# Performance work log

Hardware: AMD Instinct MI355X
Metric: run time of the kernel (lower is better)

## Reference

```python
import jax, jax.numpy as jnp
import numpy as np

B, T, I, H = 512, 512, 8, 256


def setup_inputs() -> dict:
    key = jax.random.key(0)
    ks = jax.random.split(key, 4)
    x = jax.random.normal(ks[0], (B, T, I), dtype=jnp.float32)
    W_ih = jax.random.normal(ks[1], (3 * H, I), dtype=jnp.float32) * 0.1
    W_hh = jax.random.normal(ks[2], (3 * H, H), dtype=jnp.float32) * 0.05
    b_ih = jnp.zeros((3 * H,), dtype=jnp.float32)
    b_hh = jnp.zeros((3 * H,), dtype=jnp.float32)
    W_lin = jax.random.normal(ks[3], (1, H), dtype=jnp.float32) * 0.05
    b_lin = jnp.zeros((1,), dtype=jnp.float32)
    return {"x": x, "W_ih": W_ih, "W_hh": W_hh, "b_ih": b_ih,
            "b_hh": b_hh, "W_lin": W_lin, "b_lin": b_lin,
            "pred_length": T}


def reference(x, W_ih, W_hh, b_ih, b_hh, W_lin, b_lin, pred_length):
    # GRU (pred_type='full'): emit lin_usage(h_t) at every timestep.
    Hd = W_hh.shape[1]

    def step(h, x_t):
        gi = x_t @ W_ih.T + b_ih          # [B, 3H]
        gh = h @ W_hh.T + b_hh            # [B, 3H]
        i_r, i_z, i_n = jnp.split(gi, 3, axis=-1)
        h_r, h_z, h_n = jnp.split(gh, 3, axis=-1)
        r = jax.nn.sigmoid(i_r + h_r)
        z = jax.nn.sigmoid(i_z + h_z)
        n = jnp.tanh(i_n + r * h_n)
        h_new = (1.0 - z) * n + z * h
        pred = h_new @ W_lin.T + b_lin    # [B, 1]
        return h_new, pred

    h0 = jnp.zeros((x.shape[0], Hd), dtype=x.dtype)
    _, preds = jax.lax.scan(step, h0, jnp.swapaxes(x, 0, 1))  # preds: [T, B, 1]
    return jnp.swapaxes(preds, 0, 1)                          # [B, T, 1]
```

## Files before the change

### kernel.cpp

```cpp
#include <hip/hip_runtime.h>

#define TT 512
#define II 8
#define HH 256
#define ST 296
#define RR 8
#define NB 64
#define XSR 136

typedef _Float16 h4_t  __attribute__((ext_vector_type(4)));
typedef _Float16 h8_t  __attribute__((ext_vector_type(8)));
typedef float    f32x2 __attribute__((ext_vector_type(2)));
typedef float    f32x4 __attribute__((ext_vector_type(4)));

__device__ inline h8_t cvt8(const float* __restrict__ p, float s) {
    h8_t r;
#pragma unroll
    for (int i = 0; i < 8; ++i) r[i] = (_Float16)(p[i] * s);
    return r;
}

__global__ void __launch_bounds__(512, 2) gru_kernel(
    const float* __restrict__ x,    const float* __restrict__ W_ih,
    const float* __restrict__ W_hh, const float* __restrict__ b_ih,
    const float* __restrict__ b_hh, const float* __restrict__ W_lin,
    const float* __restrict__ b_lin, float* __restrict__ out)
{
    __shared__ _Float16 hbuf[2][16][ST];
    __shared__ h8_t wz1buf[8 * 8 * 64];
    __shared__ h8_t wn1buf[8 * 8 * 64];
    __shared__ _Float16 xstage[2][RR][XSR];
    __shared__ float predbuf[2][RR][64];

    const int tid  = threadIdx.x;
    const int w    = tid >> 6;
    const int lane = tid & 63;
    const int q    = lane >> 4;
    const int r15  = lane & 15;
    const int row0 = blockIdx.x * RR;

    const float sRZ = -1.44269504088896340736f;
    const float sN  =  2.88539008177792681472f;

    const int c0 = w * 32 + r15;
    const int c1 = c0 + 16;

    h8_t wfR0[8], wfZ0[8], wfN0[8], wfR1[8];
#pragma unroll
    for (int s = 0; s < 8; ++s) {
        const int k0 = s * 32 + q * 8;
        wfR0[s] = cvt8(W_hh + (size_t)(c0)       * HH + k0, sRZ);
        wfZ0[s] = cvt8(W_hh + (size_t)(256 + c0) * HH + k0, sRZ);
        wfN0[s] = cvt8(W_hh + (size_t)(512 + c0) * HH + k0, sN);
        wfR1[s] = cvt8(W_hh + (size_t)(c1)       * HH + k0, sRZ);
        wz1buf[(w * 8 + s) * 64 + lane] = cvt8(W_hh + (size_t)(256 + c1) * HH + k0, sRZ);
        wn1buf[(w * 8 + s) * 64 + lane] = cvt8(W_hh + (size_t)(512 + c1) * HH + k0, sN);
    }
    h4_t xfR[2], xfZ[2], xfN[2];
#pragma unroll
    for (int g = 0; g < 2; ++g) {
        const int cR = g ? c1 : c0;
#pragma unroll
        for (int j = 0; j < 4; ++j) {
            const int kp = q * 4 + j;
            float vR = 0.f, vZ = 0.f, vN = 0.f;
            if (kp < 8) {
                vR = W_ih[(cR)       * II + kp] * sRZ;
                vZ = W_ih[(256 + cR) * II + kp] * sRZ;
                vN = W_ih[(512 + cR) * II + kp] * sN;
            } else if (kp == 8) {
                vR = (b_ih[cR]       + b_hh[cR])       * sRZ;
                vZ = (b_ih[256 + cR] + b_hh[256 + cR]) * sRZ;
                vN = b_ih[512 + cR] * sN;
            }
            xfR[g][j] = (_Float16)vR; xfZ[g][j] = (_Float16)vZ; xfN[g][j] = (_Float16)vN;
        }
    }
    const bool hi = (lane >= 32);
    const float bhnp = (hi ? b_hh[512 + c1] : b_hh[512 + c0]) * sN;
    const float blin = b_lin[0];
    const float wl0 = W_lin[lane * 4 + 0], wl1 = W_lin[lane * 4 + 1];
    const float wl2 = W_lin[lane * 4 + 2], wl3 = W_lin[lane * 4 + 3];

    const h4_t bias4 = {(_Float16)1.f, (_Float16)0.f, (_Float16)0.f, (_Float16)0.f};
    const h4_t zero4 = {(_Float16)0.f, (_Float16)0.f, (_Float16)0.f, (_Float16)0.f};

    for (int i = tid; i < 2 * 16 * ST; i += 512) (&hbuf[0][0][0])[i] = (_Float16)0.f;
    {
        const int rr_ = tid >> 6, f2 = (tid & 63) * 2;
        const f32x2 v = *(const f32x2*)(x + (size_t)(row0 + rr_) * TT * II + f2);
        xstage[0][rr_][f2]     = (_Float16)v[0];
        xstage[0][rr_][f2 + 1] = (_Float16)v[1];
    }
    __syncthreads();

    const h8_t* __restrict__ wz_lane = &wz1buf[w * 8 * 64 + lane];
    const h8_t* __restrict__ wn_lane = &wn1buf[w * 8 * 64 + lane];

    f32x4 hreg = {0.f, 0.f, 0.f, 0.f};
    const f32x4 z4 = {0.f, 0.f, 0.f, 0.f};

    const int rb   = (q & 1) * 4;
    const int colp = hi ? c1 : c0;

    f32x2 xpre = {0.f, 0.f};
    const int xrow = tid >> 6, xf2 = (tid & 63) * 2;

    for (int t = 0; t < TT; ++t) {
        const int cur = t & 1, nxt = cur ^ 1;
        const int win = (t >> 4) & 1;

        if ((t & 15) == 0 && t + 16 < TT) {
            xpre = *(const f32x2*)(x + ((size_t)(row0 + xrow) * TT + (t + 16)) * II + xf2);
        }

        const _Float16* hb = &hbuf[cur][r15][0];
        const h4_t xa = *(const h4_t*)&xstage[win][r15 & 7][(t & 15) * 8 + (q & 1) * 4];
        const h4_t a2 = (q < 2) ? xa : ((q == 2) ? bias4 : zero4);
        f32x4 accR0 = __builtin_amdgcn_mfma_f32_16x16x16f16(a2, xfR[0], z4, 0, 0, 0);
        f32x4 accZ0 = __builtin_amdgcn_mfma_f32_16x16x16f16(a2, xfZ[0], z4, 0, 0, 0);
        f32x4 gin0  = __builtin_amdgcn_mfma_f32_16x16x16f16(a2, xfN[0], z4, 0, 0, 0);
        f32x4 accR1 = __builtin_amdgcn_mfma_f32_16x16x16f16(a2, xfR[1], z4, 0, 0, 0);
        f32x4 accZ1 = __builtin_amdgcn_mfma_f32_16x16x16f16(a2, xfZ[1], z4, 0, 0, 0);
        f32x4 gin1  = __builtin_amdgcn_mfma_f32_16x16x16f16(a2, xfN[1], z4, 0, 0, 0);
        f32x4 accN0 = z4, accN1 = z4;
#pragma unroll
        for (int s = 0; s < 8; ++s) {
            const h8_t a  = *(const h8_t*)(hb + s * 32 + q * 8);
            const h8_t wz = wz_lane[s * 64];
            const h8_t wn = wn_lane[s * 64];
            accR0 = __builtin_amdgcn_mfma_f32_16x16x32_f16(a, wfR0[s], accR0, 0, 0, 0);
            accZ0 = __builtin_amdgcn_mfma_f32_16x16x32_f16(a, wfZ0[s], accZ0, 0, 0, 0);
            accN0 = __builtin_amdgcn_mfma_f32_16x16x32_f16(a, wfN0[s], accN0, 0, 0, 0);
            accR1 = __builtin_amdgcn_mfma_f32_16x16x32_f16(a, wfR1[s], accR1, 0, 0, 0);
            accZ1 = __builtin_amdgcn_mfma_f32_16x16x32_f16(a, wz,     accZ1, 0, 0, 0);
            accN1 = __builtin_amdgcn_mfma_f32_16x16x32_f16(a, wn,     accN1, 0, 0, 0);
        }

        if (t > 0) {
            const h4_t hv4 = *(const h4_t*)&hbuf[cur][w][lane * 4];
            float s0 = (float)hv4[0] * wl0 + (float)hv4[1] * wl1
                     + (float)hv4[2] * wl2 + (float)hv4[3] * wl3;
#pragma unroll
            for (int m = 32; m >= 1; m >>= 1) s0 += __shfl_xor(s0, m, 64);
            if (lane == 0) predbuf[((t - 1) >> 6) & 1][w][(t - 1) & 63] = s0 + blin;
        }

        _Float16* hw = &hbuf[nxt][rb][colp];
#pragma unroll
        for (int j = 0; j < 4; ++j) {
            const float vR = hi ? accR1[j] : accR0[j];
            const float vZ = hi ? accZ1[j] : accZ0[j];
            const float vN = hi ? accN1[j] : accN0[j];
            const float vG = hi ? gin1[j]  : gin0[j];
            const float rr = __builtin_amdgcn_rcpf(1.f + __builtin_amdgcn_exp2f(vR));
            const float zz = __builtin_amdgcn_rcpf(1.f + __builtin_amdgcn_exp2f(vZ));
            const float u  = vG + rr * (vN + bhnp);
            const float nn = 1.f - 2.f * __builtin_amdgcn_rcpf(1.f + __builtin_amdgcn_exp2f(u));
            const float hv = nn + zz * (hreg[j] - nn);
            hreg[j] = hv;
            const _Float16 hh = (_Float16)hv;
            hw[j * ST]          = hh;
            hw[j * ST + 8 * ST] = hh;
        }

        if ((t & 15) == 15 && t + 1 < TT) {
            _Float16* xd = &xstage[win ^ 1][xrow][xf2];
            xd[0] = (_Float16)xpre[0];
            xd[1] = (_Float16)xpre[1];
        }

        __syncthreads();

        if ((t & 63) == 0 && t > 0) {
            const int pb = ((t >> 6) & 1) ^ 1;
            out[(size_t)(row0 + (tid >> 6)) * TT + (t - 64) + (tid & 63)] =
                predbuf[pb][tid >> 6][tid & 63];
        }
    }

    {
        const h4_t hv4 = *(const h4_t*)&hbuf[TT & 1][w][lane * 4];
        float s0 = (float)hv4[0] * wl0 + (float)hv4[1] * wl1
                 + (float)hv4[2] * wl2 + (float)hv4[3] * wl3;
#pragma unroll
        for (int m = 32; m >= 1; m >>= 1) s0 += __shfl_xor(s0, m, 64);
        if (lane == 0) predbuf[1][w][63] = s0 + blin;
    }
    __syncthreads();
    out[(size_t)(row0 + (tid >> 6)) * TT + 448 + (tid & 63)] =
        predbuf[1][tid >> 6][tid & 63];
}

extern "C" void kernel_launch(void* const* d_in, const int* in_sizes, int n_in,
                              void* d_out, int out_size, void* d_ws, size_t ws_size,
                              hipStream_t stream) {
    const float* x     = (const float*)d_in[0];
    const float* W_ih  = (const float*)d_in[1];
    const float* W_hh  = (const float*)d_in[2];
    const float* b_ih  = (const float*)d_in[3];
    const float* b_hh  = (const float*)d_in[4];
    const float* W_lin = (const float*)d_in[5];
    const float* b_lin = (const float*)d_in[6];
    float* out = (float*)d_out;
    gru_kernel<<<NB, 512, 0, stream>>>(x, W_ih, W_hh, b_ih, b_hh, W_lin, b_lin, out);
}
```

Measured before the change: 886.5 us.

## Halve block to 256 threads with each wave computing 64 hidden columns

Workgroups shrink from 8 waves to 4, and each wave now processes two 32-column groups in sequence, doubling its MFMA work per step. More recurrent weights stay in registers (10 of 12 fragment sets), so fewer weights are fetched from LDS each step. The intent is to make the per-step __syncthreads cheaper with fewer waves and to cut LDS weight traffic. The cost is much higher register pressure and a longer serial MFMA chain per wave. With one block per CU and only 64 blocks, each CU holds just 4 waves, which leaves little latency hiding.

```diff
diff --git a/kernel.cpp b/kernel.cpp
--- a/kernel.cpp
+++ b/kernel.cpp
@@ -20,15 +20,15 @@
     return r;
 }
 
-__global__ void __launch_bounds__(512, 2) gru_kernel(
+__global__ void __launch_bounds__(256, 1) gru_kernel(
     const float* __restrict__ x,    const float* __restrict__ W_ih,
     const float* __restrict__ W_hh, const float* __restrict__ b_ih,
     const float* __restrict__ b_hh, const float* __restrict__ W_lin,
     const float* __restrict__ b_lin, float* __restrict__ out)
 {
     __shared__ _Float16 hbuf[2][16][ST];
-    __shared__ h8_t wz1buf[8 * 8 * 64];
-    __shared__ h8_t wn1buf[8 * 8 * 64];
+    __shared__ h8_t wn1buf[4 * 8 * 64];
+    __shared__ h8_t wn3buf[4 * 8 * 64];
     __shared__ _Float16 xstage[2][RR][XSR];
     __shared__ float predbuf[2][RR][64];
 
@@ -42,10 +42,13 @@
     const float sRZ = -1.44269504088896340736f;
     const float sN  =  2.88539008177792681472f;
 
-    const int c0 = w * 32 + r15;
+    const int c0 = w * 64 + r15;
     const int c1 = c0 + 16;
-
-    h8_t wfR0[8], wfZ0[8], wfN0[8], wfR1[8];
+    const int c2 = c0 + 32;
+    const int c3 = c0 + 48;
+
+    h8_t wfR0[8], wfZ0[8], wfN0[8], wfR1[8], wfZ1[8];
+    h8_t wfR2[8], wfZ2[8], wfN2[8], wfR3[8], wfZ3[8];
 #pragma unroll
     for (int s = 0; s < 8; ++s) {
         const int k0 = s * 32 + q * 8;
@@ -53,13 +56,20 @@
         wfZ0[s] = cvt8(W_hh + (size_t)(256 + c0) * HH + k0, sRZ);
         wfN0[s] = cvt8(W_hh + (size_t)(512 + c0) * HH + k0, sN);
         wfR1[s] = cvt8(W_hh + (size_t)(c1)       * HH + k0, sRZ);
-        wz1buf[(w * 8 + s) * 64 + lane] = cvt8(W_hh + (size_t)(256 + c1) * HH + k0, sRZ);
+        wfZ1[s] = cvt8(W_hh + (size_t)(256 + c1) * HH + k0, sRZ);
+        wfR2[s] = cvt8(W_hh + (size_t)(c2)       * HH + k0, sRZ);
+        wfZ2[s] = cvt8(W_hh + (size_t)(256 + c2) * HH + k0, sRZ);
+        wfN2[s] = cvt8(W_hh + (size_t)(512 + c2) * HH + k0, sN);
+        wfR3[s] = cvt8(W_hh + (size_t)(c3)       * HH + k0, sRZ);
+        wfZ3[s] = cvt8(W_hh + (size_t)(256 + c3) * HH + k0, sRZ);
         wn1buf[(w * 8 + s) * 64 + lane] = cvt8(W_hh + (size_t)(512 + c1) * HH + k0, sN);
-    }
-    h4_t xfR[2], xfZ[2], xfN[2];
-#pragma unroll
-    for (int g = 0; g < 2; ++g) {
-        const int cR = g ? c1 : c0;
+        wn3buf[(w * 8 + s) * 64 + lane] = cvt8(W_hh + (size_t)(512 + c3) * HH + k0, sN);
+    }
+    const int cga[4] = {c0, c1, c2, c3};
+    h4_t xfR[4], xfZ[4], xfN[4];
+#pragma unroll
+    for (int g = 0; g < 4; ++g) {
+        const int cR = cga[g];
 #pragma unroll
         for (int j = 0; j < 4; ++j) {
             const int kp = q * 4 + j;
@@ -77,119 +87,175 @@
         }
     }
     const bool hi = (lane >= 32);
-    const float bhnp = (hi ? b_hh[512 + c1] : b_hh[512 + c0]) * sN;
+    const float bhnp0 = (hi ? b_hh[512 + c1] : b_hh[512 + c0]) * sN;
+    const float bhnp1 = (hi ? b_hh[512 + c3] : b_hh[512 + c2]) * sN;
     const float blin = b_lin[0];
-    const float wl0 = W_lin[lane * 4 + 0], wl1 = W_lin[lane * 4 + 1];
-    const float wl2 = W_lin[lane * 4 + 2], wl3 = W_lin[lane * 4 + 3];
+    const int l31  = lane & 31;
+    const int prow = w + (lane >> 5) * 4;
+    float wl[8];
+#pragma unroll
+    for (int i = 0; i < 8; ++i) wl[i] = W_lin[l31 * 8 + i];
 
     const h4_t bias4 = {(_Float16)1.f, (_Float16)0.f, (_Float16)0.f, (_Float16)0.f};
     const h4_t zero4 = {(_Float16)0.f, (_Float16)0.f, (_Float16)0.f, (_Float16)0.f};
 
-    for (int i = tid; i < 2 * 16 * ST; i += 512) (&hbuf[0][0][0])[i] = (_Float16)0.f;
+    for (int i = tid; i < 2 * 16 * ST; i += 256) (&hbuf[0][0][0])[i] = (_Float16)0.f;
+    const int xrow = tid >> 5, xf4 = (tid & 31) * 4;
     {
-        const int rr_ = tid >> 6, f2 = (tid & 63) * 2;
-        const f32x2 v = *(const f32x2*)(x + (size_t)(row0 + rr_) * TT * II + f2);
-        xstage[0][rr_][f2]     = (_Float16)v[0];
-        xstage[0][rr_][f2 + 1] = (_Float16)v[1];
+        const f32x4 v = *(const f32x4*)(x + (size_t)(row0 + xrow) * TT * II + xf4);
+        xstage[0][xrow][xf4]     = (_Float16)v[0];
+        xstage[0][xrow][xf4 + 1] = (_Float16)v[1];
+        xstage[0][xrow][xf4 + 2] = (_Float16)v[2];
+        xstage[0][xrow][xf4 + 3] = (_Float16)v[3];
     }
     __syncthreads();
 
-    const h8_t* __restrict__ wz_lane = &wz1buf[w * 8 * 64 + lane];
-    const h8_t* __restrict__ wn_lane = &wn1buf[w * 8 * 64 + lane];
-
-    f32x4 hreg = {0.f, 0.f, 0.f, 0.f};
+    const h8_t* __restrict__ wn1_lane = &wn1buf[w * 8 * 64 + lane];
+    const h8_t* __restrict__ wn3_lane = &wn3buf[w * 8 * 64 + lane];
+
+    f32x4 hreg0 = {0.f, 0.f, 0.f, 0.f};
+    f32x4 hreg1 = {0.f, 0.f, 0.f, 0.f};
     const f32x4 z4 = {0.f, 0.f, 0.f, 0.f};
 
-    const int rb   = (q & 1) * 4;
-    const int colp = hi ? c1 : c0;
-
-    f32x2 xpre = {0.f, 0.f};
-    const int xrow = tid >> 6, xf2 = (tid & 63) * 2;
+    const int rb = (q & 1) * 4;
+    f32x4 xpre = {0.f, 0.f, 0.f, 0.f};
 
     for (int t = 0; t < TT; ++t) {
         const int cur = t & 1, nxt = cur ^ 1;
         const int win = (t >> 4) & 1;
 
         if ((t & 15) == 0 && t + 16 < TT) {
-            xpre = *(const f32x2*)(x + ((size_t)(row0 + xrow) * TT + (t + 16)) * II + xf2);
-        }
-
-        const _Float16* hb = &hbuf[cur][r15][0];
+            xpre = *(const f32x4*)(x + ((size_t)(row0 + xrow) * TT + (t + 16)) * II + xf4);
+        }
+
         const h4_t xa = *(const h4_t*)&xstage[win][r15 & 7][(t & 15) * 8 + (q & 1) * 4];
         const h4_t a2 = (q < 2) ? xa : ((q == 2) ? bias4 : zero4);
-        f32x4 accR0 = __builtin_amdgcn_mfma_f32_16x16x16f16(a2, xfR[0], z4, 0, 0, 0);
-        f32x4 accZ0 = __builtin_amdgcn_mfma_f32_16x16x16f16(a2, xfZ[0], z4, 0, 0, 0);
-        f32x4 gin0  = __builtin_amdgcn_mfma_f32_16x16x16f16(a2, xfN[0], z4, 0, 0, 0);
-        f32x4 accR1 = __builtin_amdgcn_mfma_f32_16x16x16f16(a2, xfR[1], z4, 0, 0, 0);
-        f32x4 accZ1 = __builtin_amdgcn_mfma_f32_16x16x16f16(a2, xfZ[1], z4, 0, 0, 0);
-        f32x4 gin1  = __builtin_amdgcn_mfma_f32_16x16x16f16(a2, xfN[1], z4, 0, 0, 0);
-        f32x4 accN0 = z4, accN1 = z4;
-#pragma unroll
-        for (int s = 0; s < 8; ++s) {
-            const h8_t a  = *(const h8_t*)(hb + s * 32 + q * 8);
-            const h8_t wz = wz_lane[s * 64];
-            const h8_t wn = wn_lane[s * 64];
-            accR0 = __builtin_amdgcn_mfma_f32_16x16x32_f16(a, wfR0[s], accR0, 0, 0, 0);
-            accZ0 = __builtin_amdgcn_mfma_f32_16x16x32_f16(a, wfZ0[s], accZ0, 0, 0, 0);
-            accN0 = __builtin_amdgcn_mfma_f32_16x16x32_f16(a, wfN0[s], accN0, 0, 0, 0);
-            accR1 = __builtin_amdgcn_mfma_f32_16x16x32_f16(a, wfR1[s], accR1, 0, 0, 0);
-            accZ1 = __builtin_amdgcn_mfma_f32_16x16x32_f16(a, wz,     accZ1, 0, 0, 0);
-            accN1 = __builtin_amdgcn_mfma_f32_16x16x32_f16(a, wn,     accN1, 0, 0, 0);
+
+        {
+            const _Float16* hb = &hbuf[cur][r15][0];
+            f32x4 aR0 = __builtin_amdgcn_mfma_f32_16x16x16f16(a2, xfR[0], z4, 0, 0, 0);
+            f32x4 aZ0 = __builtin_amdgcn_mfma_f32_16x16x16f16(a2, xfZ[0], z4, 0, 0, 0);
+            f32x4 gi0 = __builtin_amdgcn_mfma_f32_16x16x16f16(a2, xfN[0], z4, 0, 0, 0);
+            f32x4 aR1 = __builtin_amdgcn_mfma_f32_16x16x16f16(a2, xfR[1], z4, 0, 0, 0);
+            f32x4 aZ1 = __builtin_amdgcn_mfma_f32_16x16x16f16(a2, xfZ[1], z4, 0, 0, 0);
+            f32x4 gi1 = __builtin_amdgcn_mfma_f32_16x16x16f16(a2, xfN[1], z4, 0, 0, 0);
+            f32x4 aN0 = z4, aN1 = z4;
+#pragma unroll
+            for (int s = 0; s < 8; ++s) {
+                const h8_t a  = *(const h8_t*)(hb + s * 32 + q * 8);
+                const h8_t wn = wn1_lane[s * 64];
+                aR0 = __builtin_amdgcn_mfma_f32_16x16x32_f16(a, wfR0[s], aR0, 0, 0, 0);
+                aZ0 = __builtin_amdgcn_mfma_f32_16x16x32_f16(a, wfZ0[s], aZ0, 0, 0, 0);
+                aN0 = __builtin_amdgcn_mfma_f32_16x16x32_f16(a, wfN0[s], aN0, 0, 0, 0);
+                aR1 = __builtin_amdgcn_mfma_f32_16x16x32_f16(a, wfR1[s], aR1, 0, 0, 0);
+                aZ1 = __builtin_amdgcn_mfma_f32_16x16x32_f16(a, wfZ1[s], aZ1, 0, 0, 0);
+                aN1 = __builtin_amdgcn_mfma_f32_16x16x32_f16(a, wn,     aN1, 0, 0, 0);
+            }
+            _Float16* hw = &hbuf[nxt][rb][hi ? c1 : c0];
+#pragma unroll
+            for (int j = 0; j < 4; ++j) {
+                const float vR = hi ? aR1[j] : aR0[j];
+                const float vZ = hi ? aZ1[j] : aZ0[j];
+                const float vN = hi ? aN1[j] : aN0[j];
+                const float vG = hi ? gi1[j] : gi0[j];
+                const float rr = __builtin_amdgcn_rcpf(1.f + __builtin_amdgcn_exp2f(vR));
+                const float zz = __builtin_amdgcn_rcpf(1.f + __builtin_amdgcn_exp2f(vZ));
+                const float u  = vG + rr * (vN + bhnp0);
+                const float nn = 1.f - 2.f * __builtin_amdgcn_rcpf(1.f + __builtin_amdgcn_exp2f(u));
+                const float hv = nn + zz * (hreg0[j] - nn);
+                hreg0[j] = hv;
+                const _Float16 hh = (_Float16)hv;
+                hw[j * ST]          = hh;
+                hw[j * ST + 8 * ST] = hh;
+            }
         }
 
         if (t > 0) {
-            const h4_t hv4 = *(const h4_t*)&hbuf[cur][w][lane * 4];
-            float s0 = (float)hv4[0] * wl0 + (float)hv4[1] * wl1
-                     + (float)hv4[2] * wl2 + (float)hv4[3] * wl3;
-#pragma unroll
-            for (int m = 32; m >= 1; m >>= 1) s0 += __shfl_xor(s0, m, 64);
-            if (lane == 0) predbuf[((t - 1) >> 6) & 1][w][(t - 1) & 63] = s0 + blin;
-        }
-
-        _Float16* hw = &hbuf[nxt][rb][colp];
-#pragma unroll
-        for (int j = 0; j < 4; ++j) {
-            const float vR = hi ? accR1[j] : accR0[j];
-            const float vZ = hi ? accZ1[j] : accZ0[j];
-            const float vN = hi ? accN1[j] : accN0[j];
-            const float vG = hi ? gin1[j]  : gin0[j];
-            const float rr = __builtin_amdgcn_rcpf(1.f + __builtin_amdgcn_exp2f(vR));
-            const float zz = __builtin_amdgcn_rcpf(1.f + __builtin_amdgcn_exp2f(vZ));
-            const float u  = vG + rr * (vN + bhnp);
-            const float nn = 1.f - 2.f * __builtin_amdgcn_rcpf(1.f + __builtin_amdgcn_exp2f(u));
-            const float hv = nn + zz * (hreg[j] - nn);
-            hreg[j] = hv;
-            const _Float16 hh = (_Float16)hv;
-            hw[j * ST]          = hh;
-            hw[j * ST + 8 * ST] = hh;
+            const h8_t hv8 = *(const h8_t*)&hbuf[cur][prow][l31 * 8];
+            float s0 = 0.f;
+#pragma unroll
+            for (int i = 0; i < 8; ++i) s0 += (float)hv8[i] * wl[i];
+#pragma unroll
+            for (int m = 16; m >= 1; m >>= 1) s0 += __shfl_xor(s0, m, 64);
+            if (l31 == 0) predbuf[((t - 1) >> 6) & 1][prow][(t - 1) & 63] = s0 + blin;
+        }
+
+        {
+            const _Float16* hb = &hbuf[cur][r15 ^ 8][0];
+            f32x4 aR2 = __builtin_amdgcn_mfma_f32_16x16x16f16(a2, xfR[2], z4, 0, 0, 0);
+            f32x4 aZ2 = __builtin_amdgcn_mfma_f32_16x16x16f16(a2, xfZ[2], z4, 0, 0, 0);
+            f32x4 gi2 = __builtin_amdgcn_mfma_f32_16x16x16f16(a2, xfN[2], z4, 0, 0, 0);
+            f32x4 aR3 = __builtin_amdgcn_mfma_f32_16x16x16f16(a2, xfR[3], z4, 0, 0, 0);
+            f32x4 aZ3 = __builtin_amdgcn_mfma_f32_16x16x16f16(a2, xfZ[3], z4, 0, 0, 0);
+            f32x4 gi3 = __builtin_amdgcn_mfma_f32_16x16x16f16(a2, xfN[3], z4, 0, 0, 0);
+            f32x4 aN2 = z4, aN3 = z4;
+#pragma unroll
+            for (int s = 0; s < 8; ++s) {
+                const h8_t a  = *(const h8_t*)(hb + s * 32 + q * 8);
+                const h8_t wn = wn3_lane[s * 64];
+                aR2 = __builtin_amdgcn_mfma_f32_16x16x32_f16(a, wfR2[s], aR2, 0, 0, 0);
+                aZ2 = __builtin_amdgcn_mfma_f32_16x16x32_f16(a, wfZ2[s], aZ2, 0, 0, 0);
+                aN2 = __builtin_amdgcn_mfma_f32_16x16x32_f16(a, wfN2[s], aN2, 0, 0, 0);
+                aR3 = __builtin_amdgcn_mfma_f32_16x16x32_f16(a, wfR3[s], aR3, 0, 0, 0);
+                aZ3 = __builtin_amdgcn_mfma_f32_16x16x32_f16(a, wfZ3[s], aZ3, 0, 0, 0);
+                aN3 = __builtin_amdgcn_mfma_f32_16x16x32_f16(a, wn,     aN3, 0, 0, 0);
+            }
+            _Float16* hw = &hbuf[nxt][rb][hi ? c3 : c2];
+#pragma unroll
+            for (int j = 0; j < 4; ++j) {
+                const float vR = hi ? aR3[j] : aR2[j];
+                const float vZ = hi ? aZ3[j] : aZ2[j];
+                const float vN = hi ? aN3[j] : aN2[j];
+                const float vG = hi ? gi3[j] : gi2[j];
+                const float rr = __builtin_amdgcn_rcpf(1.f + __builtin_amdgcn_exp2f(vR));
+                const float zz = __builtin_amdgcn_rcpf(1.f + __builtin_amdgcn_exp2f(vZ));
+                const float u  = vG + rr * (vN + bhnp1);
+                const float nn = 1.f - 2.f * __builtin_amdgcn_rcpf(1.f + __builtin_amdgcn_exp2f(u));
+                const float hv = nn + zz * (hreg1[j] - nn);
+                hreg1[j] = hv;
+                const _Float16 hh = (_Float16)hv;
+                hw[j * ST]          = hh;
+                hw[j * ST + 8 * ST] = hh;
+            }
         }
 
         if ((t & 15) == 15 && t + 1 < TT) {
-            _Float16* xd = &xstage[win ^ 1][xrow][xf2];
+            _Float16* xd = &xstage[win ^ 1][xrow][xf4];
             xd[0] = (_Float16)xpre[0];
             xd[1] = (_Float16)xpre[1];
+            xd[2] = (_Float16)xpre[2];
+            xd[3] = (_Float16)xpre[3];
         }
 
         __syncthreads();
 
         if ((t & 63) == 0 && t > 0) {
             const int pb = ((t >> 6) & 1) ^ 1;
-            out[(size_t)(row0 + (tid >> 6)) * TT + (t - 64) + (tid & 63)] =
-                predbuf[pb][tid >> 6][tid & 63];
+            const int pr = tid >> 5, cc = (tid & 31) * 2;
+            f32x2 pv;
+            pv[0] = predbuf[pb][pr][cc];
+            pv[1] = predbuf[pb][pr][cc + 1];
+            *(f32x2*)&out[(size_t)(row0 + pr) * TT + (t - 64) + cc] = pv;
         }
     }
 
     {
-        const h4_t hv4 = *(const h4_t*)&hbuf[TT & 1][w][lane * 4];
-        float s0 = (float)hv4[0] * wl0 + (float)hv4[1] * wl1
-                 + (float)hv4[2] * wl2 + (float)hv4[3] * wl3;
-#pragma unroll
-        for (int m = 32; m >= 1; m >>= 1) s0 += __shfl_xor(s0, m, 64);
-        if (lane == 0) predbuf[1][w][63] = s0 + blin;
+        const h8_t hv8 = *(const h8_t*)&hbuf[TT & 1][prow][l31 * 8];
+        float s0 = 0.f;
+#pragma unroll
+        for (int i = 0; i < 8; ++i) s0 += (float)hv8[i] * wl[i];
+#pragma unroll
+        for (int m = 16; m >= 1; m >>= 1) s0 += __shfl_xor(s0, m, 64);
+        if (l31 == 0) predbuf[1][prow][63] = s0 + blin;
     }
     __syncthreads();
-    out[(size_t)(row0 + (tid >> 6)) * TT + 448 + (tid & 63)] =
-        predbuf[1][tid >> 6][tid & 63];
+    {
+        const int pr = tid >> 5, cc = (tid & 31) * 2;
+        f32x2 pv;
+        pv[0] = predbuf[1][pr][cc];
+        pv[1] = predbuf[1][pr][cc + 1];
+        *(f32x2*)&out[(size_t)(row0 + pr) * TT + 448 + cc] = pv;
+    }
 }
 
 extern "C" void kernel_launch(void* const* d_in, const int* in_sizes, int n_in,
@@ -203,5 +269,5 @@
     const float* W_lin = (const float*)d_in[5];
     const float* b_lin = (const float*)d_in[6];
     float* out = (float*)d_out;
-    gru_kernel<<<NB, 512, 0, stream>>>(x, W_ih, W_hh, b_ih, b_hh, W_lin, b_lin, out);
+    gru_kernel<<<NB, 256, 0, stream>>>(x, W_ih, W_hh, b_ih, b_hh, W_lin, b_lin, out);
 }
```

Measured after the change: 1.242 ms. +40.1%, slower.
